# Performance work log

Hardware: AMD Instinct MI355X
Metric: run time of the kernel (lower is better)

The kernel has to match this reference:

```python
import jax, jax.numpy as jnp
import numpy as np

N = 100000
E = 1600000
NODE_DIM = 64
H = 128
NUM_LAYERS = 3
NUM_CLASSES = 6
NUM_GRAPHS = 512
LN_EPS = 1e-5


def setup_inputs() -> dict:
    key = jax.random.key(0)
    ks = jax.random.split(key, 16)
    s = 0.05
    x = jax.random.normal(ks[0], (N, NODE_DIM), jnp.float32)
    edge_index = jax.random.randint(ks[1], (2, E), 0, N, dtype=jnp.int64)
    batch = jnp.sort(jax.random.randint(ks[2], (N,), 0, NUM_GRAPHS, dtype=jnp.int64))
    return {
        "x": x,
        "edge_index": edge_index,
        "batch": batch,
        "proj_w": jax.random.normal(ks[3], (NODE_DIM, H), jnp.float32) * s,
        "proj_b": jnp.zeros((H,), jnp.float32),
        "lin_l_w": jax.random.normal(ks[4], (NUM_LAYERS, H, H), jnp.float32) * s,
        "lin_l_b": jnp.zeros((NUM_LAYERS, H), jnp.float32),
        "lin_r_w": jax.random.normal(ks[5], (NUM_LAYERS, H, H), jnp.float32) * s,
        "ln_g": jnp.ones((NUM_LAYERS, H), jnp.float32),
        "ln_b": jnp.zeros((NUM_LAYERS, H), jnp.float32),
        "gate_w1": jax.random.normal(ks[6], (H, H // 2), jnp.float32) * s,
        "gate_b1": jnp.zeros((H // 2,), jnp.float32),
        "gate_w2": jax.random.normal(ks[7], (H // 2, 1), jnp.float32) * s,
        "gate_b2": jnp.zeros((1,), jnp.float32),
        "cls_w1": jax.random.normal(ks[8], (H, H // 2), jnp.float32) * s,
        "cls_b1": jnp.zeros((H // 2,), jnp.float32),
        "cls_w2": jax.random.normal(ks[9], (H // 2, NUM_CLASSES), jnp.float32) * s,
        "cls_b2": jnp.zeros((NUM_CLASSES,), jnp.float32),
    }


def _layer_norm(x, g, b):
    mu = jnp.mean(x, axis=-1, keepdims=True)
    var = jnp.mean(jnp.square(x - mu), axis=-1, keepdims=True)
    return (x - mu) * jax.lax.rsqrt(var + LN_EPS) * g + b


def _sage_mean_aggr(x, src, dst):
    # mean of source node features grouped by destination node
    summed = jax.ops.segment_sum(x[src], dst, num_segments=N)  # [N,H]
    deg = jax.ops.segment_sum(jnp.ones((E,), x.dtype), dst, num_segments=N)
    return summed / jnp.maximum(deg, 1.0)[:, None]


def reference(x, edge_index, batch, proj_w, proj_b, lin_l_w, lin_l_b, lin_r_w,
              ln_g, ln_b, gate_w1, gate_b1, gate_w2, gate_b2,
              cls_w1, cls_b1, cls_w2, cls_b2):
    src, dst = edge_index[0], edge_index[1]
    h = jax.nn.relu(x @ proj_w + proj_b)  # [N,H]
    for l in range(NUM_LAYERS):
        r = h
        aggr = _sage_mean_aggr(h, src, dst)
        # PyG SAGEConv: lin_l(aggregated) + lin_r(self), bias only in lin_l
        h = aggr @ lin_l_w[l] + lin_l_b[l] + h @ lin_r_w[l]
        h = _layer_norm(h, ln_g[l], ln_b[l])
        h = jax.nn.elu(h)
        h = h + r  # dropout is identity in eval mode
    # GlobalAttention pooling: segment softmax over nodes per graph
    gate = (jax.nn.relu(h @ gate_w1 + gate_b1) @ gate_w2 + gate_b2)[:, 0]  # [N]
    gmax = jax.ops.segment_max(gate, batch, num_segments=NUM_GRAPHS)
    eg = jnp.exp(gate - gmax[batch])
    denom = jax.ops.segment_sum(eg, batch, num_segments=NUM_GRAPHS)
    alpha = eg / denom[batch]  # [N]
    pooled = jax.ops.segment_sum(h * alpha[:, None], batch, num_segments=NUM_GRAPHS)  # [G,H]
    out = jax.nn.relu(pooled @ cls_w1 + cls_b1) @ cls_w2 + cls_b2  # [G,C]
    return out
```

## Files before the change

### kernel.cpp

```cpp
#include <hip/hip_runtime.h>
#include <hip/hip_fp16.h>
#include <math.h>

#define N_NODES   100000
#define N_EDGES   1600000
#define NDIM      64
#define H         128
#define NUM_LAYERS 3
#define NUM_CLASSES 6
#define NUM_GRAPHS 512
#define LN_EPS    1e-5f
#define NBKT      391
#define SCAP      5376
#define BPAD      136

typedef _Float16 f16x8 __attribute__((ext_vector_type(8)));
typedef float    f32x4 __attribute__((ext_vector_type(4)));

__device__ __forceinline__ int idx_at(const int* raw, int is64, int i) {
    return is64 ? raw[2 * (long long)i] : raw[i];
}
__device__ __forceinline__ int lower_bound(const int* a, int n, int v) {
    int lo = 0, hi = n;
    while (lo < hi) { int m = (lo + hi) >> 1; if (a[m] < v) lo = m + 1; else hi = m; }
    return lo;
}

__device__ __forceinline__ f32x4 gload16(const __half* __restrict__ base, int voff) {
    f32x4 r;
    asm volatile("global_load_dwordx4 %0, %1, %2"
                 : "=v"(r) : "v"(voff), "s"(base));
    return r;
}

__global__ void k_detect(const int* eraw, const int* braw, int* flags,
                         int* bcnt, float* gate_z) {
    int i = blockIdx.x * blockDim.x + threadIdx.x;
    if (i < 512) bcnt[i] = 0;
    if (i < 64) gate_z[i] = 0.f;
    if (i == 0) {
        int e64 = 1;
        for (int k = 1; k < 128; k += 2) if (eraw[k] != 0) { e64 = 0; break; }
        flags[0] = e64;
        flags[1] = (braw[N_NODES - 1] == 0) ? 1 : 0;
    }
}

__global__ __launch_bounds__(256) void k_bhist(const int* eraw, const int* braw,
                                               const int* flags, int* bcnt, int* batch32) {
    __shared__ int c[512];
    int tid = threadIdx.x;
    for (int i = tid; i < 512; i += 256) c[i] = 0;
    __syncthreads();
    int f = flags[0];
    int gi = blockIdx.x * 256 + tid;
    if (gi < N_NODES) batch32[gi] = idx_at(braw, flags[1], gi);
    int stride = gridDim.x * 256;
    for (int e = blockIdx.x * 256 + tid; e < N_EDGES; e += stride) {
        int d = idx_at(eraw, f, N_EDGES + e);
        atomicAdd(&c[d >> 8], 1);
    }
    __syncthreads();
    for (int i = tid; i < 512; i += 256) if (c[i]) atomicAdd(&bcnt[i], c[i]);
}

__global__ void k_bscan(const int* bcnt, int* boff, int* bcursor) {
    __shared__ int sh[512];
    int tid = threadIdx.x;
    int v = bcnt[tid];
    sh[tid] = v;
    __syncthreads();
    for (int off = 1; off < 512; off <<= 1) {
        int u = (tid >= off) ? sh[tid - off] : 0;
        __syncthreads();
        sh[tid] += u;
        __syncthreads();
    }
    int excl = sh[tid] - v;
    boff[tid] = excl;
    bcursor[tid] = excl;
    if (tid == 511) boff[512] = sh[511];
}

#define EPB 4096
__global__ __launch_bounds__(256) void k_bucket(const int* eraw, const int* flags,
                                                int* bcursor, unsigned int* br) {
    __shared__ int cnt[512];
    __shared__ int excl[512];
    __shared__ int resv[512];
    __shared__ int lcur[512];
    __shared__ int psum[256];
    __shared__ unsigned int srec[EPB];
    __shared__ unsigned short sbkt[EPB];
    int tid = threadIdx.x;
    int f = flags[0];
    int base = blockIdx.x * EPB;
    int se[16], de[16];
#pragma unroll
    for (int j = 0; j < 16; ++j) {
        int e = base + j * 256 + tid;
        if (e < N_EDGES) {
            se[j] = idx_at(eraw, f, e);
            de[j] = idx_at(eraw, f, N_EDGES + e);
        } else de[j] = -1;
    }
    for (int i = tid; i < 512; i += 256) cnt[i] = 0;
    __syncthreads();
#pragma unroll
    for (int j = 0; j < 16; ++j)
        if (de[j] >= 0) atomicAdd(&cnt[de[j] >> 8], 1);
    __syncthreads();
    int b0 = cnt[2 * tid], b1 = cnt[2 * tid + 1];
    psum[tid] = b0 + b1;
    __syncthreads();
    for (int off = 1; off < 256; off <<= 1) {
        int u = (tid >= off) ? psum[tid - off] : 0;
        __syncthreads();
        psum[tid] += u;
        __syncthreads();
    }
    int pex = psum[tid] - (b0 + b1);
    excl[2 * tid] = pex;
    excl[2 * tid + 1] = pex + b0;
    lcur[2 * tid] = pex;
    lcur[2 * tid + 1] = pex + b0;
    resv[2 * tid]     = b0 ? atomicAdd(&bcursor[2 * tid], b0) : 0;
    resv[2 * tid + 1] = b1 ? atomicAdd(&bcursor[2 * tid + 1], b1) : 0;
    __syncthreads();
#pragma unroll
    for (int j = 0; j < 16; ++j)
        if (de[j] >= 0) {
            int b = de[j] >> 8;
            int slot = atomicAdd(&lcur[b], 1);
            srec[slot] = ((unsigned int)(de[j] & 255) << 24) | (unsigned int)se[j];
            sbkt[slot] = (unsigned short)b;
        }
    __syncthreads();
    int vtot = psum[255];
    for (int s2 = tid; s2 < vtot; s2 += 256) {
        int b = sbkt[s2];
        br[resv[b] + (s2 - excl[b])] = srec[s2];
    }
}

__global__ __launch_bounds__(256) void k_csr_tail(const unsigned int* br, const int* boff,
                                                  int* rowptr, int* col) {
    __shared__ int d256[256];
    __shared__ int sc[256];
    __shared__ int cbuf[SCAP];
    int b = blockIdx.x;
    int tid = threadIdx.x;
    int lo = boff[b], hi = boff[b + 1];
    int wsize = hi - lo;
    d256[tid] = 0;
    __syncthreads();
    for (int i = lo + tid; i < hi; i += 256)
        atomicAdd(&d256[br[i] >> 24], 1);
    __syncthreads();
    int v = d256[tid];
    sc[tid] = v;
    __syncthreads();
    for (int off = 1; off < 256; off <<= 1) {
        int u = (tid >= off) ? sc[tid - off] : 0;
        __syncthreads();
        sc[tid] += u;
        __syncthreads();
    }
    int excl = sc[tid] - v;
    int node = (b << 8) + tid;
    if (node < N_NODES) rowptr[node] = lo + excl;
    if (b == NBKT - 1 && tid == 0) rowptr[N_NODES] = N_EDGES;
    __syncthreads();
    d256[tid] = excl;
    __syncthreads();
    if (wsize <= SCAP) {
        for (int i = lo + tid; i < hi; i += 256) {
            unsigned int r = br[i];
            int p = atomicAdd(&d256[r >> 24], 1);
            cbuf[p] = (int)(r & 0xFFFFFF);
        }
        __syncthreads();
        for (int j = tid; j < wsize; j += 256) col[lo + j] = cbuf[j] << 8;
    } else {
        for (int i = lo + tid; i < hi; i += 256) {
            unsigned int r = br[i];
            int p = atomicAdd(&d256[r >> 24], 1);
            col[lo + p] = (int)(r & 0xFFFFFF) << 8;
        }
    }
}

__global__ void k_prepw(const float* __restrict__ lin_l_w, const float* __restrict__ lin_r_w,
                        const float* __restrict__ gate_w1,
                        __half* __restrict__ W16t, __half* __restrict__ W16g) {
    int i = blockIdx.x * 256 + threadIdx.x;
    if (i < NUM_LAYERS * 128 * 256) {
        int l = i >> 15;
        int rem = i & 32767;
        int n = rem >> 8;
        int k = rem & 255;
        float v = (k < 128) ? lin_l_w[(size_t)l * 16384 + k * 128 + n]
                            : lin_r_w[(size_t)l * 16384 + (k - 128) * 128 + n];
        W16t[(size_t)l * 32768 + n * 256 + k] = __float2half(v);
    } else if (i < NUM_LAYERS * 128 * 256 + 64 * 128) {
        int idx = i - NUM_LAYERS * 128 * 256;
        int n = idx >> 7;
        int k = idx & 127;
        W16g[n * 128 + k] = __float2half(gate_w1[k * 64 + n]);
    }
}

__global__ __launch_bounds__(256) void k_gemm_proj(const float* __restrict__ A,
                                                   const float* __restrict__ W,
                                                   const float* __restrict__ bias,
                                                   __half* __restrict__ C16,
                                                   int nrows, int K) {
    __shared__ float As_t[32][68];
    __shared__ float Ws[32 * 128];
    int tid = threadIdx.x;
    int row0 = blockIdx.x * 64;
    int tr = tid >> 4;
    int tc = tid & 15;
    int c0 = tc * 8;
    float acc[4][8];
#pragma unroll
    for (int i = 0; i < 4; ++i)
#pragma unroll
        for (int j = 0; j < 8; ++j) acc[i][j] = 0.f;

    for (int kc = 0; kc < K; kc += 32) {
        __syncthreads();
#pragma unroll
        for (int it = 0; it < 2; ++it) {
            int idx = tid + it * 256;
            int r = idx >> 3, c4 = idx & 7;
            int gr = row0 + r;
            float4 v = make_float4(0.f, 0.f, 0.f, 0.f);
            if (gr < nrows) v = *(const float4*)(A + (size_t)gr * K + kc + c4 * 4);
            As_t[c4 * 4 + 0][r] = v.x;
            As_t[c4 * 4 + 1][r] = v.y;
            As_t[c4 * 4 + 2][r] = v.z;
            As_t[c4 * 4 + 3][r] = v.w;
        }
#pragma unroll
        for (int it = 0; it < 4; ++it) {
            int idx = tid + it * 256;
            int r = idx >> 5, c4 = idx & 31;
            *(float4*)(&Ws[r * 128 + c4 * 4]) = *(const float4*)(W + (size_t)(kc + r) * 128 + c4 * 4);
        }
        __syncthreads();
#pragma unroll
        for (int k = 0; k < 32; ++k) {
            float4 a4 = *(const float4*)(&As_t[k][tr * 4]);
            float a[4] = {a4.x, a4.y, a4.z, a4.w};
            float4 w0 = *(const float4*)(&Ws[k * 128 + c0]);
            float4 w1 = *(const float4*)(&Ws[k * 128 + c0 + 4]);
            float w[8] = {w0.x, w0.y, w0.z, w0.w, w1.x, w1.y, w1.z, w1.w};
#pragma unroll
            for (int i = 0; i < 4; ++i)
#pragma unroll
                for (int j = 0; j < 8; ++j) acc[i][j] += a[i] * w[j];
        }
    }
    float bv[8];
#pragma unroll
    for (int j = 0; j < 8; ++j) bv[j] = bias[c0 + j];
#pragma unroll
    for (int i = 0; i < 4; ++i) {
        int gr = row0 + tr * 4 + i;
        if (gr < nrows) {
            float o[8];
#pragma unroll
            for (int j = 0; j < 8; ++j) o[j] = fmaxf(acc[i][j] + bv[j], 0.f);
            __half2 p[4];
#pragma unroll
            for (int j = 0; j < 8; j += 2) p[j / 2] = __floats2half2_rn(o[j], o[j + 1]);
            *(float4*)(C16 + (size_t)gr * 128 + c0) = *(float4*)p;
        }
    }
}

__global__ __launch_bounds__(256) void k_layer_mfma(const __half* __restrict__ t16,
                                                    __half* __restrict__ h16,
                                                    const __half* __restrict__ W16t,
                                                    const float* __restrict__ bl,
                                                    const float* __restrict__ g,
                                                    const float* __restrict__ bb) {
    __shared__ __half Bs[128 * BPAD];
    int tid = threadIdx.x;
    int wave = tid >> 6, lane = tid & 63;
    int s = lane & 15, quad = lane >> 4;
    int row0 = blockIdx.x * 64;
    int wrow0 = row0 + wave * 16;
    int arow = wrow0 + s;
    if (arow >= N_NODES) arow = N_NODES - 1;

    f32x4 acc[8];
#pragma unroll
    for (int c = 0; c < 8; ++c) acc[c] = (f32x4){0.f, 0.f, 0.f, 0.f};

#pragma unroll
    for (int ph = 0; ph < 2; ++ph) {
        __syncthreads();
#pragma unroll
        for (int it = 0; it < 8; ++it) {
            int idx = tid + it * 256;
            int n = idx >> 4, ch = idx & 15;
            *(float4*)(&Bs[n * BPAD + ch * 8]) =
                *(const float4*)(W16t + (size_t)n * 256 + ph * 128 + ch * 8);
        }
        __syncthreads();
        const __half* aptr = (ph ? h16 : t16) + (size_t)arow * H;
#pragma unroll
        for (int kk = 0; kk < 128; kk += 32) {
            f16x8 afrag = *(const f16x8*)(aptr + kk + quad * 8);
#pragma unroll
            for (int c = 0; c < 8; ++c) {
                f16x8 bfrag = *(const f16x8*)(&Bs[(c * 16 + s) * BPAD + kk + quad * 8]);
                acc[c] = __builtin_amdgcn_mfma_f32_16x16x32_f16(afrag, bfrag, acc[c], 0, 0, 0);
            }
        }
    }

    float y[8][4];
    float sm[4] = {0.f, 0.f, 0.f, 0.f}, sq[4] = {0.f, 0.f, 0.f, 0.f};
#pragma unroll
    for (int c = 0; c < 8; ++c) {
        float bv = bl[c * 16 + s];
#pragma unroll
        for (int i = 0; i < 4; ++i) {
            float v = acc[c][i] + bv;
            y[c][i] = v;
            sm[i] += v;
            sq[i] += v * v;
        }
    }
#pragma unroll
    for (int off = 1; off < 16; off <<= 1) {
#pragma unroll
        for (int i = 0; i < 4; ++i) {
            sm[i] += __shfl_xor(sm[i], off);
            sq[i] += __shfl_xor(sq[i], off);
        }
    }
    float mean[4], rstd[4];
#pragma unroll
    for (int i = 0; i < 4; ++i) {
        mean[i] = sm[i] * (1.0f / H);
        float var = sq[i] * (1.0f / H) - mean[i] * mean[i];
        rstd[i] = rsqrtf(var + LN_EPS);
    }
    float gv[8], bbv[8];
#pragma unroll
    for (int c = 0; c < 8; ++c) { gv[c] = g[c * 16 + s]; bbv[c] = bb[c * 16 + s]; }

    __syncthreads();
#pragma unroll
    for (int i = 0; i < 4; ++i) {
        int lr = wave * 16 + quad * 4 + i;
#pragma unroll
        for (int c = 0; c < 8; ++c) {
            float yv = (y[c][i] - mean[i]) * rstd[i] * gv[c] + bbv[c];
            yv = yv > 0.f ? yv : expf(yv) - 1.f;
            Bs[lr * BPAD + c * 16 + s] = __float2half(yv);
        }
    }
    __syncthreads();
#pragma unroll
    for (int it = 0; it < 4; ++it) {
        int idx = tid + it * 256;
        int r = idx >> 4, ch = idx & 15;
        int grow = row0 + r;
        if (grow < N_NODES) {
            float4 sv = *(float4*)(&Bs[r * BPAD + ch * 8]);
            float4 hv = *(const float4*)(h16 + (size_t)grow * H + ch * 8);
            __half2* pa = (__half2*)&sv;
            const __half2* pb = (const __half2*)&hv;
#pragma unroll
            for (int j = 0; j < 4; ++j) {
                float2 fa = __half22float2(pa[j]);
                float2 fb = __half22float2(pb[j]);
                pa[j] = __floats2half2_rn(fa.x + fb.x, fa.y + fb.y);
            }
            *(float4*)(h16 + (size_t)grow * H + ch * 8) = sv;
        }
    }
}

__global__ __launch_bounds__(256) void k_layer_gate(const __half* __restrict__ t16,
                                                    __half* __restrict__ h16,
                                                    const __half* __restrict__ W16t,
                                                    const float* __restrict__ bl,
                                                    const float* __restrict__ g,
                                                    const float* __restrict__ bb,
                                                    const __half* __restrict__ W16g,
                                                    const float* __restrict__ gb1,
                                                    const float* __restrict__ gw2,
                                                    const float* __restrict__ gb2,
                                                    float* __restrict__ gateout) {
    __shared__ __half Bs[128 * BPAD];
    int tid = threadIdx.x;
    int wave = tid >> 6, lane = tid & 63;
    int s = lane & 15, quad = lane >> 4;
    int row0 = blockIdx.x * 64;
    int wrow0 = row0 + wave * 16;
    int arow = wrow0 + s;
    if (arow >= N_NODES) arow = N_NODES - 1;

    f32x4 acc[8];
#pragma unroll
    for (int c = 0; c < 8; ++c) acc[c] = (f32x4){0.f, 0.f, 0.f, 0.f};

#pragma unroll
    for (int ph = 0; ph < 2; ++ph) {
        __syncthreads();
#pragma unroll
        for (int it = 0; it < 8; ++it) {
            int idx = tid + it * 256;
            int n = idx >> 4, ch = idx & 15;
            *(float4*)(&Bs[n * BPAD + ch * 8]) =
                *(const float4*)(W16t + (size_t)n * 256 + ph * 128 + ch * 8);
        }
        __syncthreads();
        const __half* aptr = (ph ? h16 : t16) + (size_t)arow * H;
#pragma unroll
        for (int kk = 0; kk < 128; kk += 32) {
            f16x8 afrag = *(const f16x8*)(aptr + kk + quad * 8);
#pragma unroll
            for (int c = 0; c < 8; ++c) {
                f16x8 bfrag = *(const f16x8*)(&Bs[(c * 16 + s) * BPAD + kk + quad * 8]);
                acc[c] = __builtin_amdgcn_mfma_f32_16x16x32_f16(afrag, bfrag, acc[c], 0, 0, 0);
            }
        }
    }

    float y[8][4];
    float sm[4] = {0.f, 0.f, 0.f, 0.f}, sq[4] = {0.f, 0.f, 0.f, 0.f};
#pragma unroll
    for (int c = 0; c < 8; ++c) {
        float bv = bl[c * 16 + s];
#pragma unroll
        for (int i = 0; i < 4; ++i) {
            float v = acc[c][i] + bv;
            y[c][i] = v;
            sm[i] += v;
            sq[i] += v * v;
        }
    }
#pragma unroll
    for (int off = 1; off < 16; off <<= 1) {
#pragma unroll
        for (int i = 0; i < 4; ++i) {
            sm[i] += __shfl_xor(sm[i], off);
            sq[i] += __shfl_xor(sq[i], off);
        }
    }
    float mean[4], rstd[4];
#pragma unroll
    for (int i = 0; i < 4; ++i) {
        mean[i] = sm[i] * (1.0f / H);
        float var = sq[i] * (1.0f / H) - mean[i] * mean[i];
        rstd[i] = rsqrtf(var + LN_EPS);
    }
    float gv[8], bbv[8];
#pragma unroll
    for (int c = 0; c < 8; ++c) { gv[c] = g[c * 16 + s]; bbv[c] = bb[c * 16 + s]; }

    __syncthreads();
#pragma unroll
    for (int i = 0; i < 4; ++i) {
        int lr = wave * 16 + quad * 4 + i;
#pragma unroll
        for (int c = 0; c < 8; ++c) {
            float yv = (y[c][i] - mean[i]) * rstd[i] * gv[c] + bbv[c];
            yv = yv > 0.f ? yv : expf(yv) - 1.f;
            Bs[lr * BPAD + c * 16 + s] = __float2half(yv);
        }
    }
    __syncthreads();
#pragma unroll
    for (int it = 0; it < 4; ++it) {
        int idx = tid + it * 256;
        int r = idx >> 4, ch = idx & 15;
        int grow = row0 + r;
        if (grow < N_NODES) {
            float4 sv = *(float4*)(&Bs[r * BPAD + ch * 8]);
            float4 hv = *(const float4*)(h16 + (size_t)grow * H + ch * 8);
            __half2* pa = (__half2*)&sv;
            const __half2* pb = (const __half2*)&hv;
#pragma unroll
            for (int j = 0; j < 4; ++j) {
                float2 fa = __half22float2(pa[j]);
                float2 fb = __half22float2(pb[j]);
                pa[j] = __floats2half2_rn(fa.x + fb.x, fa.y + fb.y);
            }
            *(float4*)(h16 + (size_t)grow * H + ch * 8) = sv;
        }
    }

    __syncthreads();
#pragma unroll
    for (int it = 0; it < 4; ++it) {
        int idx = tid + it * 256;
        int n = idx >> 4, ch = idx & 15;
        *(float4*)(&Bs[n * BPAD + ch * 8]) = *(const float4*)(W16g + (size_t)n * 128 + ch * 8);
    }
    __syncthreads();
    f32x4 gacc[4];
#pragma unroll
    for (int c = 0; c < 4; ++c) gacc[c] = (f32x4){0.f, 0.f, 0.f, 0.f};
    const __half* gaptr = h16 + (size_t)arow * H;
#pragma unroll
    for (int kc = 0; kc < 128; kc += 32) {
        f16x8 afrag = *(const f16x8*)(gaptr + kc + quad * 8);
#pragma unroll
        for (int c = 0; c < 4; ++c) {
            f16x8 bfrag = *(const f16x8*)(&Bs[(c * 16 + s) * BPAD + kc + quad * 8]);
            gacc[c] = __builtin_amdgcn_mfma_f32_16x16x32_f16(afrag, bfrag, gacc[c], 0, 0, 0);
        }
    }
    float part[4] = {0.f, 0.f, 0.f, 0.f};
#pragma unroll
    for (int c = 0; c < 4; ++c) {
        float bv = gb1[c * 16 + s];
        float wv = gw2[c * 16 + s];
#pragma unroll
        for (int i = 0; i < 4; ++i)
            part[i] += fmaxf(gacc[c][i] + bv, 0.f) * wv;
    }
#pragma unroll
    for (int off = 1; off < 16; off <<= 1) {
#pragma unroll
        for (int i = 0; i < 4; ++i) part[i] += __shfl_xor(part[i], off);
    }
    if (s == 0) {
        float b2v = gb2[0];
#pragma unroll
        for (int i = 0; i < 4; ++i) {
            int r = wrow0 + quad * 4 + i;
            if (r < N_NODES) gateout[r] = part[i] + b2v;
        }
    }
}

__global__ __launch_bounds__(256) void k_aggr(const __half* __restrict__ h16,
                                              const int* __restrict__ rowptr,
                                              const int* __restrict__ col,
                                              __half* __restrict__ t16,
                                              int zoff) {
    int lane = threadIdx.x & 63;
    int node = blockIdx.x * 4 + (threadIdx.x >> 6);
    if (node >= N_NODES) return;
    int s = lane & 15;
    int g = lane >> 4;
    int soff = s * 16;
    int e0 = rowptr[node];
    int deg = rowptr[node + 1] - e0;

    if (deg == 0) {
        if (g == 0) {
            float4 zz = make_float4(0.f, 0.f, 0.f, 0.f);
            *(float4*)(t16 + (size_t)node * H + s * 8) = zz;
        }
        return;
    }

    __half2 z = __floats2half2_rn(0.f, 0.f);
    __half2 ac[4][4];
#pragma unroll
    for (int a = 0; a < 4; ++a)
#pragma unroll
        for (int k = 0; k < 4; ++k) ac[a][k] = z;

    {
        int cb[8];
#pragma unroll
        for (int j = 0; j < 8; ++j) {
            int ei = g + 4 * j;
            cb[j] = col[e0 + (ei < deg ? ei : 0)];
        }
#pragma unroll
        for (int j = 0; j < 8; ++j) {
            int ei = g + 4 * j;
            cb[j] = ((ei < deg) ? cb[j] : zoff) + soff;
        }
        __builtin_amdgcn_sched_barrier(0);
        f32x4 rv[8];
#pragma unroll
        for (int j = 0; j < 8; ++j) rv[j] = gload16(h16, cb[j]);
        asm volatile("s_waitcnt vmcnt(0)" ::: "memory");
        __builtin_amdgcn_sched_barrier(0);
#pragma unroll
        for (int j = 0; j < 8; ++j) {
            const __half2* hv = (const __half2*)&rv[j];
            int a = j & 3;
            ac[a][0] = __hadd2(ac[a][0], hv[0]);
            ac[a][1] = __hadd2(ac[a][1], hv[1]);
            ac[a][2] = __hadd2(ac[a][2], hv[2]);
            ac[a][3] = __hadd2(ac[a][3], hv[3]);
        }
    }

    if (deg > 32) {
        for (int base = 32; base < deg; base += 32) {
            int cb[8];
#pragma unroll
            for (int j = 0; j < 8; ++j) {
                int ei = base + g + 4 * j;
                cb[j] = col[e0 + (ei < deg ? ei : base)];
            }
#pragma unroll
            for (int j = 0; j < 8; ++j) {
                int ei = base + g + 4 * j;
                cb[j] = ((ei < deg) ? cb[j] : zoff) + soff;
            }
            __builtin_amdgcn_sched_barrier(0);
            f32x4 rv[8];
#pragma unroll
            for (int j = 0; j < 8; ++j) rv[j] = gload16(h16, cb[j]);
            asm volatile("s_waitcnt vmcnt(0)" ::: "memory");
            __builtin_amdgcn_sched_barrier(0);
#pragma unroll
            for (int j = 0; j < 8; ++j) {
                const __half2* hv = (const __half2*)&rv[j];
                int a = j & 3;
                ac[a][0] = __hadd2(ac[a][0], hv[0]);
                ac[a][1] = __hadd2(ac[a][1], hv[1]);
                ac[a][2] = __hadd2(ac[a][2], hv[2]);
                ac[a][3] = __hadd2(ac[a][3], hv[3]);
            }
        }
    }

    float f[8];
#pragma unroll
    for (int k = 0; k < 4; ++k) {
        float2 s0 = __half22float2(ac[0][k]);
        float2 s1 = __half22float2(ac[1][k]);
        float2 s2 = __half22float2(ac[2][k]);
        float2 s3 = __half22float2(ac[3][k]);
        f[2 * k]     = (s0.x + s1.x) + (s2.x + s3.x);
        f[2 * k + 1] = (s0.y + s1.y) + (s2.y + s3.y);
    }
#pragma unroll
    for (int off = 16; off <= 32; off <<= 1) {
#pragma unroll
        for (int k = 0; k < 8; ++k) f[k] += __shfl_xor(f[k], off);
    }
    if (g == 0) {
        float inv = 1.0f / (float)(deg > 1 ? deg : 1);
        __half2 o[4];
#pragma unroll
        for (int k = 0; k < 4; ++k)
            o[k] = __floats2half2_rn(f[2 * k] * inv, f[2 * k + 1] * inv);
        *(float4*)(t16 + (size_t)node * H + s * 8) = *(float4*)o;
    }
}

__global__ __launch_bounds__(256) void k_smx_pool_cls(const __half* __restrict__ h16,
                                                      const float* __restrict__ gatein,
                                                      const int* __restrict__ batch32,
                                                      const float* __restrict__ w1,
                                                      const float* __restrict__ b1,
                                                      const float* __restrict__ w2,
                                                      const float* __restrict__ b2,
                                                      float* __restrict__ out) {
    __shared__ float seg[512];
    __shared__ float red[256];
    __shared__ float smem[256 * 8];
    __shared__ float sp[64];
    int g = blockIdx.x;
    int tid = threadIdx.x;
    int n0 = lower_bound(batch32, N_NODES, g);
    int n1 = lower_bound(batch32, N_NODES, g + 1);
    int cnt = n1 - n0;
    int cc = cnt < 512 ? cnt : 512;

    float g0 = (tid < cc) ? gatein[n0 + tid] : -INFINITY;
    float g1 = (256 + tid < cc) ? gatein[n0 + 256 + tid] : -INFINITY;
    red[tid] = fmaxf(g0, g1);
    __syncthreads();
    for (int st = 128; st >= 1; st >>= 1) {
        if (tid < st) red[tid] = fmaxf(red[tid], red[tid + st]);
        __syncthreads();
    }
    float m = red[0];
    __syncthreads();
    float e0 = (tid < cc) ? expf(g0 - m) : 0.f;
    float e1 = (256 + tid < cc) ? expf(g1 - m) : 0.f;
    if (tid < cc) seg[tid] = e0;
    if (256 + tid < cc) seg[256 + tid] = e1;
    red[tid] = e0 + e1;
    __syncthreads();
    for (int st = 128; st >= 1; st >>= 1) {
        if (tid < st) red[tid] += red[tid + st];
        __syncthreads();
    }
    float gs = red[0];
    __syncthreads();

    int c8 = tid & 15, p = tid >> 4;
    float f[8];
#pragma unroll
    for (int j = 0; j < 8; ++j) f[j] = 0.f;
    for (int ln = p; ln < cc; ln += 16) {
        float4 v = *(const float4*)(h16 + (size_t)(n0 + ln) * H + c8 * 8);
        const __half2* hv = (const __half2*)&v;
        float w = seg[ln];
#pragma unroll
        for (int j = 0; j < 4; ++j) {
            float2 fv = __half22float2(hv[j]);
            f[2 * j]     += w * fv.x;
            f[2 * j + 1] += w * fv.y;
        }
    }
#pragma unroll
    for (int j = 0; j < 8; ++j) smem[tid * 8 + j] = f[j];
    __syncthreads();
    for (int st = 8; st >= 1; st >>= 1) {
        if (p < st) {
#pragma unroll
            for (int j = 0; j < 8; ++j)
                smem[tid * 8 + j] += smem[(tid + st * 16) * 8 + j];
        }
        __syncthreads();
    }
    if (p == 0) {
#pragma unroll
        for (int j = 0; j < 8; ++j)
            red[c8 * 8 + j] = (cnt > 0) ? smem[c8 * 8 + j] / gs : 0.f;
    }
    __syncthreads();

    if (tid < 64) {
        float r0 = red[tid];
        float r1 = red[64 + tid];
        float acc = b1[tid];
#pragma unroll 16
        for (int k = 0; k < 64; ++k) acc += __shfl(r0, k) * w1[k * 64 + tid];
#pragma unroll 16
        for (int k = 0; k < 64; ++k) acc += __shfl(r1, k) * w1[(64 + k) * 64 + tid];
        sp[tid] = fmaxf(acc, 0.f);
    }
    __syncthreads();
    if (tid < NUM_CLASSES) {
        float o = b2[tid];
        for (int c = 0; c < 64; ++c) o += sp[c] * w2[c * NUM_CLASSES + tid];
        out[g * NUM_CLASSES + tid] = o;
    }
}

extern "C" void kernel_launch(void* const* d_in, const int* in_sizes, int n_in,
                              void* d_out, int out_size, void* d_ws, size_t ws_size,
                              hipStream_t stream) {
    const float* x       = (const float*)d_in[0];
    const int*   eraw    = (const int*)d_in[1];
    const int*   braw    = (const int*)d_in[2];
    const float* proj_w  = (const float*)d_in[3];
    const float* proj_b  = (const float*)d_in[4];
    const float* lin_l_w = (const float*)d_in[5];
    const float* lin_l_b = (const float*)d_in[6];
    const float* lin_r_w = (const float*)d_in[7];
    const float* ln_g    = (const float*)d_in[8];
    const float* ln_b    = (const float*)d_in[9];
    const float* gate_w1 = (const float*)d_in[10];
    const float* gate_b1 = (const float*)d_in[11];
    const float* gate_w2 = (const float*)d_in[12];
    const float* gate_b2 = (const float*)d_in[13];
    const float* cls_w1  = (const float*)d_in[14];
    const float* cls_b1  = (const float*)d_in[15];
    const float* cls_w2  = (const float*)d_in[16];
    const float* cls_b2  = (const float*)d_in[17];
    float* out = (float*)d_out;

    __half* h16    = (__half*)d_ws;
    __half* t16    = h16 + (size_t)N_NODES * H;
    float*  gate   = (float*)(t16 + (size_t)N_NODES * H);
    float*  gsum   = gate + N_NODES;
    float*  pooled = gsum + NUM_GRAPHS;
    __half* W16t   = (__half*)(pooled + NUM_GRAPHS * H);
    __half* W16g   = W16t + (size_t)NUM_LAYERS * 32768;
    int* flags     = (int*)(W16g + 64 * 128);
    int* col       = flags + 4;
    int* batch32   = col + N_EDGES;
    int* rowptr    = batch32 + N_NODES;
    int* bcnt      = rowptr + N_NODES + 1;
    int* boff      = bcnt + 512;
    int* bcursor   = boff + 513;
    unsigned int* br = (unsigned int*)(bcursor + 512);

    const int zoff = (int)((const char*)gate - (const char*)h16);

    const int nbE4 = (N_EDGES + EPB - 1) / EPB;
    const int nbW = (N_NODES + 3) / 4;
    const int nbG = (N_NODES + 63) / 64;
    const int nbP = (NUM_LAYERS * 128 * 256 + 64 * 128 + 255) / 256;

    k_detect<<<2, 256, 0, stream>>>(eraw, braw, flags, bcnt, gate);
    k_bhist<<<512, 256, 0, stream>>>(eraw, braw, flags, bcnt, batch32);
    k_bscan<<<1, 512, 0, stream>>>(bcnt, boff, bcursor);
    k_bucket<<<nbE4, 256, 0, stream>>>(eraw, flags, bcursor, br);
    k_csr_tail<<<NBKT, 256, 0, stream>>>(br, boff, rowptr, col);
    k_prepw<<<nbP, 256, 0, stream>>>(lin_l_w, lin_r_w, gate_w1, W16t, W16g);

    k_gemm_proj<<<nbG, 256, 0, stream>>>(x, proj_w, proj_b, h16, N_NODES, NDIM);

    for (int l = 0; l < NUM_LAYERS; ++l) {
        const float* bl  = lin_l_b + (size_t)l * H;
        const float* gl  = ln_g + (size_t)l * H;
        const float* blb = ln_b + (size_t)l * H;
        k_aggr<<<nbW, 256, 0, stream>>>(h16, rowptr, col, t16, zoff);
        if (l < NUM_LAYERS - 1) {
            k_layer_mfma<<<nbG, 256, 0, stream>>>(t16, h16, W16t + (size_t)l * 32768, bl, gl, blb);
        } else {
            k_layer_gate<<<nbG, 256, 0, stream>>>(t16, h16, W16t + (size_t)l * 32768, bl, gl, blb,
                                                  W16g, gate_b1, gate_w2, gate_b2, gate);
        }
    }

    k_smx_pool_cls<<<NUM_GRAPHS, 256, 0, stream>>>(h16, gate, batch32,
                                                   cls_w1, cls_b1, cls_w2, cls_b2, out);
}
```

Before: 457.7 us.

## Store node features in column-sliced planar layout and slice aggregation by feature chunk

New measurement: 608.6 us. 1.33x slower.

```diff
diff --git a/kernel.cpp b/kernel.cpp
--- a/kernel.cpp
+++ b/kernel.cpp
@@ -13,6 +13,7 @@
 #define NBKT      391
 #define SCAP      5376
 #define BPAD      136
+#define PLH32     (N_NODES * 16)
 
 typedef _Float16 f16x8 __attribute__((ext_vector_type(8)));
 typedef float    f32x4 __attribute__((ext_vector_type(4)));
@@ -25,10 +26,13 @@
     while (lo < hi) { int m = (lo + hi) >> 1; if (a[m] < v) lo = m + 1; else hi = m; }
     return lo;
 }
-
-__device__ __forceinline__ f32x4 gload16(const __half* __restrict__ base, int voff) {
-    f32x4 r;
-    asm volatile("global_load_dwordx4 %0, %1, %2"
+__device__ __forceinline__ size_t pmoff(int c, int n) {
+    return (size_t)(c >> 1) * PLH32 + (size_t)n * 16 + (size_t)((c & 1) * 8);
+}
+
+__device__ __forceinline__ float2 gload8(const __half* __restrict__ base, int voff) {
+    float2 r;
+    asm volatile("global_load_dwordx2 %0, %1, %2"
                  : "=v"(r) : "v"(voff), "s"(base));
     return r;
 }
@@ -180,12 +184,12 @@
             cbuf[p] = (int)(r & 0xFFFFFF);
         }
         __syncthreads();
-        for (int j = tid; j < wsize; j += 256) col[lo + j] = cbuf[j] << 8;
+        for (int j = tid; j < wsize; j += 256) col[lo + j] = cbuf[j] << 5;
     } else {
         for (int i = lo + tid; i < hi; i += 256) {
             unsigned int r = br[i];
             int p = atomicAdd(&d256[r >> 24], 1);
-            col[lo + p] = (int)(r & 0xFFFFFF) << 8;
+            col[lo + p] = (int)(r & 0xFFFFFF) << 5;
         }
     }
 }
@@ -275,7 +279,7 @@
             __half2 p[4];
 #pragma unroll
             for (int j = 0; j < 8; j += 2) p[j / 2] = __floats2half2_rn(o[j], o[j + 1]);
-            *(float4*)(C16 + (size_t)gr * 128 + c0) = *(float4*)p;
+            *(float4*)(C16 + pmoff(tc, gr)) = *(float4*)p;
         }
     }
 }
@@ -310,10 +314,10 @@
                 *(const float4*)(W16t + (size_t)n * 256 + ph * 128 + ch * 8);
         }
         __syncthreads();
-        const __half* aptr = (ph ? h16 : t16) + (size_t)arow * H;
+        const __half* aptr = ph ? h16 : t16;
 #pragma unroll
         for (int kk = 0; kk < 128; kk += 32) {
-            f16x8 afrag = *(const f16x8*)(aptr + kk + quad * 8);
+            f16x8 afrag = *(const f16x8*)(aptr + pmoff(kk / 8 + quad, arow));
 #pragma unroll
             for (int c = 0; c < 8; ++c) {
                 f16x8 bfrag = *(const f16x8*)(&Bs[(c * 16 + s) * BPAD + kk + quad * 8]);
@@ -369,11 +373,11 @@
 #pragma unroll
     for (int it = 0; it < 4; ++it) {
         int idx = tid + it * 256;
-        int r = idx >> 4, ch = idx & 15;
+        int r = idx & 63, ch = idx >> 6;
         int grow = row0 + r;
         if (grow < N_NODES) {
             float4 sv = *(float4*)(&Bs[r * BPAD + ch * 8]);
-            float4 hv = *(const float4*)(h16 + (size_t)grow * H + ch * 8);
+            float4 hv = *(const float4*)(h16 + pmoff(ch, grow));
             __half2* pa = (__half2*)&sv;
             const __half2* pb = (const __half2*)&hv;
 #pragma unroll
@@ -382,7 +386,7 @@
                 float2 fb = __half22float2(pb[j]);
                 pa[j] = __floats2half2_rn(fa.x + fb.x, fa.y + fb.y);
             }
-            *(float4*)(h16 + (size_t)grow * H + ch * 8) = sv;
+            *(float4*)(h16 + pmoff(ch, grow)) = sv;
         }
     }
 }
@@ -422,10 +426,10 @@
                 *(const float4*)(W16t + (size_t)n * 256 + ph * 128 + ch * 8);
         }
         __syncthreads();
-        const __half* aptr = (ph ? h16 : t16) + (size_t)arow * H;
+        const __half* aptr = ph ? h16 : t16;
 #pragma unroll
         for (int kk = 0; kk < 128; kk += 32) {
-            f16x8 afrag = *(const f16x8*)(aptr + kk + quad * 8);
+            f16x8 afrag = *(const f16x8*)(aptr + pmoff(kk / 8 + quad, arow));
 #pragma unroll
             for (int c = 0; c < 8; ++c) {
                 f16x8 bfrag = *(const f16x8*)(&Bs[(c * 16 + s) * BPAD + kk + quad * 8]);
@@ -481,11 +485,11 @@
 #pragma unroll
     for (int it = 0; it < 4; ++it) {
         int idx = tid + it * 256;
-        int r = idx >> 4, ch = idx & 15;
+        int r = idx & 63, ch = idx >> 6;
         int grow = row0 + r;
         if (grow < N_NODES) {
             float4 sv = *(float4*)(&Bs[r * BPAD + ch * 8]);
-            float4 hv = *(const float4*)(h16 + (size_t)grow * H + ch * 8);
+            float4 hv = *(const float4*)(h16 + pmoff(ch, grow));
             __half2* pa = (__half2*)&sv;
             const __half2* pb = (const __half2*)&hv;
 #pragma unroll
@@ -494,7 +498,7 @@
                 float2 fb = __half22float2(pb[j]);
                 pa[j] = __floats2half2_rn(fa.x + fb.x, fa.y + fb.y);
             }
-            *(float4*)(h16 + (size_t)grow * H + ch * 8) = sv;
+            *(float4*)(h16 + pmoff(ch, grow)) = sv;
         }
     }
 
@@ -509,10 +513,9 @@
     f32x4 gacc[4];
 #pragma unroll
     for (int c = 0; c < 4; ++c) gacc[c] = (f32x4){0.f, 0.f, 0.f, 0.f};
-    const __half* gaptr = h16 + (size_t)arow * H;
 #pragma unroll
     for (int kc = 0; kc < 128; kc += 32) {
-        f16x8 afrag = *(const f16x8*)(gaptr + kc + quad * 8);
+        f16x8 afrag = *(const f16x8*)(h16 + pmoff(kc / 8 + quad, arow));
 #pragma unroll
         for (int c = 0; c < 4; ++c) {
             f16x8 bfrag = *(const f16x8*)(&Bs[(c * 16 + s) * BPAD + kc + quad * 8]);
@@ -548,112 +551,104 @@
                                               const int* __restrict__ col,
                                               __half* __restrict__ t16,
                                               int zoff) {
-    int lane = threadIdx.x & 63;
-    int node = blockIdx.x * 4 + (threadIdx.x >> 6);
-    if (node >= N_NODES) return;
-    int s = lane & 15;
-    int g = lane >> 4;
-    int soff = s * 16;
-    int e0 = rowptr[node];
-    int deg = rowptr[node + 1] - e0;
-
-    if (deg == 0) {
-        if (g == 0) {
-            float4 zz = make_float4(0.f, 0.f, 0.f, 0.f);
-            *(float4*)(t16 + (size_t)node * H + s * 8) = zz;
-        }
-        return;
-    }
-
-    __half2 z = __floats2half2_rn(0.f, 0.f);
-    __half2 ac[4][4];
-#pragma unroll
-    for (int a = 0; a < 4; ++a)
-#pragma unroll
-        for (int k = 0; k < 4; ++k) ac[a][k] = z;
-
-    {
-        int cb[8];
-#pragma unroll
-        for (int j = 0; j < 8; ++j) {
-            int ei = g + 4 * j;
-            cb[j] = col[e0 + (ei < deg ? ei : 0)];
-        }
-#pragma unroll
-        for (int j = 0; j < 8; ++j) {
-            int ei = g + 4 * j;
-            cb[j] = ((ei < deg) ? cb[j] : zoff) + soff;
-        }
+    int tid = threadIdx.x;
+    int slice = blockIdx.x & 7;
+    int nb = blockIdx.x >> 3;
+    int lane = tid & 63;
+    int e = lane >> 2, q = lane & 3;
+    int pq = slice * (N_NODES * 32) + q * 8;
+    char* tb = (char*)t16 + slice * (N_NODES * 32) + q * 8;
+    int nbase = nb * 256 + (tid >> 6) * 64;
+
+    for (int itn = 0; itn < 16; ++itn) {
+        int n0 = nbase + itn * 4;
+        if (n0 >= N_NODES) return;
+        int4 rp = *(const int4*)(rowptr + n0);
+        int rp4 = rowptr[n0 + 4];
+        int d0 = rp.y - rp.x, d1 = rp.z - rp.y, d2 = rp.w - rp.z, d3 = rp4 - rp.w;
+        int i0 = e, i1 = 16 + e;
+        int c0 = col[rp.x + (i0 < d0 ? i0 : 0)];
+        int c1 = col[rp.x + (i1 < d0 ? i1 : 0)];
+        int c2 = col[rp.y + (i0 < d1 ? i0 : 0)];
+        int c3 = col[rp.y + (i1 < d1 ? i1 : 0)];
+        int c4 = col[rp.z + (i0 < d2 ? i0 : 0)];
+        int c5 = col[rp.z + (i1 < d2 ? i1 : 0)];
+        int c6 = col[rp.w + (i0 < d3 ? i0 : 0)];
+        int c7 = col[rp.w + (i1 < d3 ? i1 : 0)];
+        int v0 = (i0 < d0) ? c0 + pq : zoff;
+        int v1 = (i1 < d0) ? c1 + pq : zoff;
+        int v2 = (i0 < d1) ? c2 + pq : zoff;
+        int v3 = (i1 < d1) ? c3 + pq : zoff;
+        int v4 = (i0 < d2) ? c4 + pq : zoff;
+        int v5 = (i1 < d2) ? c5 + pq : zoff;
+        int v6 = (i0 < d3) ? c6 + pq : zoff;
+        int v7 = (i1 < d3) ? c7 + pq : zoff;
         __builtin_amdgcn_sched_barrier(0);
-        f32x4 rv[8];
-#pragma unroll
-        for (int j = 0; j < 8; ++j) rv[j] = gload16(h16, cb[j]);
+        float2 g0 = gload8(h16, v0);
+        float2 g1 = gload8(h16, v1);
+        float2 g2 = gload8(h16, v2);
+        float2 g3 = gload8(h16, v3);
+        float2 g4 = gload8(h16, v4);
+        float2 g5 = gload8(h16, v5);
+        float2 g6 = gload8(h16, v6);
+        float2 g7 = gload8(h16, v7);
         asm volatile("s_waitcnt vmcnt(0)" ::: "memory");
         __builtin_amdgcn_sched_barrier(0);
-#pragma unroll
-        for (int j = 0; j < 8; ++j) {
-            const __half2* hv = (const __half2*)&rv[j];
-            int a = j & 3;
-            ac[a][0] = __hadd2(ac[a][0], hv[0]);
-            ac[a][1] = __hadd2(ac[a][1], hv[1]);
-            ac[a][2] = __hadd2(ac[a][2], hv[2]);
-            ac[a][3] = __hadd2(ac[a][3], hv[3]);
-        }
-    }
-
-    if (deg > 32) {
-        for (int base = 32; base < deg; base += 32) {
-            int cb[8];
-#pragma unroll
-            for (int j = 0; j < 8; ++j) {
-                int ei = base + g + 4 * j;
-                cb[j] = col[e0 + (ei < deg ? ei : base)];
+
+        __half2 al[4], ah[4];
+        {
+            const __half2* p0 = (const __half2*)&g0;
+            const __half2* p1 = (const __half2*)&g1;
+            al[0] = __hadd2(p0[0], p1[0]); ah[0] = __hadd2(p0[1], p1[1]);
+            const __half2* p2 = (const __half2*)&g2;
+            const __half2* p3 = (const __half2*)&g3;
+            al[1] = __hadd2(p2[0], p3[0]); ah[1] = __hadd2(p2[1], p3[1]);
+            const __half2* p4 = (const __half2*)&g4;
+            const __half2* p5 = (const __half2*)&g5;
+            al[2] = __hadd2(p4[0], p5[0]); ah[2] = __hadd2(p4[1], p5[1]);
+            const __half2* p6 = (const __half2*)&g6;
+            const __half2* p7 = (const __half2*)&g7;
+            al[3] = __hadd2(p6[0], p7[0]); ah[3] = __hadd2(p6[1], p7[1]);
+        }
+
+        if ((d0 > 32) | (d1 > 32) | (d2 > 32) | (d3 > 32)) {
+            int dd0[4] = {d0, d1, d2, d3};
+            int ee0[4] = {rp.x, rp.y, rp.z, rp.w};
+#pragma unroll
+            for (int j = 0; j < 4; ++j) {
+                for (int base = 32; base < dd0[j]; base += 16) {
+                    int ii = base + e;
+                    int cc = col[ee0[j] + (ii < dd0[j] ? ii : 0)];
+                    int vv = (ii < dd0[j]) ? cc + pq : zoff;
+                    float2 gg = gload8(h16, vv);
+                    asm volatile("s_waitcnt vmcnt(0)" ::: "memory");
+                    const __half2* pg = (const __half2*)&gg;
+                    al[j] = __hadd2(al[j], pg[0]);
+                    ah[j] = __hadd2(ah[j], pg[1]);
+                }
             }
-#pragma unroll
-            for (int j = 0; j < 8; ++j) {
-                int ei = base + g + 4 * j;
-                cb[j] = ((ei < deg) ? cb[j] : zoff) + soff;
+        }
+
+        int dd[4] = {d0, d1, d2, d3};
+#pragma unroll
+        for (int j = 0; j < 4; ++j) {
+#pragma unroll
+            for (int off = 4; off <= 32; off <<= 1) {
+                int tl = __shfl_xor(*(int*)&al[j], off);
+                int th = __shfl_xor(*(int*)&ah[j], off);
+                al[j] = __hadd2(al[j], *(__half2*)&tl);
+                ah[j] = __hadd2(ah[j], *(__half2*)&th);
             }
-            __builtin_amdgcn_sched_barrier(0);
-            f32x4 rv[8];
-#pragma unroll
-            for (int j = 0; j < 8; ++j) rv[j] = gload16(h16, cb[j]);
-            asm volatile("s_waitcnt vmcnt(0)" ::: "memory");
-            __builtin_amdgcn_sched_barrier(0);
-#pragma unroll
-            for (int j = 0; j < 8; ++j) {
-                const __half2* hv = (const __half2*)&rv[j];
-                int a = j & 3;
-                ac[a][0] = __hadd2(ac[a][0], hv[0]);
-                ac[a][1] = __hadd2(ac[a][1], hv[1]);
-                ac[a][2] = __hadd2(ac[a][2], hv[2]);
-                ac[a][3] = __hadd2(ac[a][3], hv[3]);
+            if (e == 0) {
+                float2 fl = __half22float2(al[j]);
+                float2 fh = __half22float2(ah[j]);
+                float inv = 1.0f / (float)(dd[j] > 1 ? dd[j] : 1);
+                float2 ov;
+                ((__half2*)&ov)[0] = __floats2half2_rn(fl.x * inv, fl.y * inv);
+                ((__half2*)&ov)[1] = __floats2half2_rn(fh.x * inv, fh.y * inv);
+                *(float2*)(tb + (size_t)(n0 + j) * 32) = ov;
             }
         }
-    }
-
-    float f[8];
-#pragma unroll
-    for (int k = 0; k < 4; ++k) {
-        float2 s0 = __half22float2(ac[0][k]);
-        float2 s1 = __half22float2(ac[1][k]);
-        float2 s2 = __half22float2(ac[2][k]);
-        float2 s3 = __half22float2(ac[3][k]);
-        f[2 * k]     = (s0.x + s1.x) + (s2.x + s3.x);
-        f[2 * k + 1] = (s0.y + s1.y) + (s2.y + s3.y);
-    }
-#pragma unroll
-    for (int off = 16; off <= 32; off <<= 1) {
-#pragma unroll
-        for (int k = 0; k < 8; ++k) f[k] += __shfl_xor(f[k], off);
-    }
-    if (g == 0) {
-        float inv = 1.0f / (float)(deg > 1 ? deg : 1);
-        __half2 o[4];
-#pragma unroll
-        for (int k = 0; k < 4; ++k)
-            o[k] = __floats2half2_rn(f[2 * k] * inv, f[2 * k + 1] * inv);
-        *(float4*)(t16 + (size_t)node * H + s * 8) = *(float4*)o;
     }
 }
 
@@ -704,7 +699,7 @@
 #pragma unroll
     for (int j = 0; j < 8; ++j) f[j] = 0.f;
     for (int ln = p; ln < cc; ln += 16) {
-        float4 v = *(const float4*)(h16 + (size_t)(n0 + ln) * H + c8 * 8);
+        float4 v = *(const float4*)(h16 + pmoff(c8, n0 + ln));
         const __half2* hv = (const __half2*)&v;
         float w = seg[ln];
 #pragma unroll
@@ -792,7 +787,7 @@
     const int zoff = (int)((const char*)gate - (const char*)h16);
 
     const int nbE4 = (N_EDGES + EPB - 1) / EPB;
-    const int nbW = (N_NODES + 3) / 4;
+    const int nbA = 8 * NBKT;
     const int nbG = (N_NODES + 63) / 64;
     const int nbP = (NUM_LAYERS * 128 * 256 + 64 * 128 + 255) / 256;
 
@@ -809,7 +804,7 @@
         const float* bl  = lin_l_b + (size_t)l * H;
         const float* gl  = ln_g + (size_t)l * H;
         const float* blb = ln_b + (size_t)l * H;
-        k_aggr<<<nbW, 256, 0, stream>>>(h16, rowptr, col, t16, zoff);
+        k_aggr<<<nbA, 256, 0, stream>>>(h16, rowptr, col, t16, zoff);
         if (l < NUM_LAYERS - 1) {
             k_layer_mfma<<<nbG, 256, 0, stream>>>(t16, h16, W16t + (size_t)l * 32768, bl, gl, blb);
         } else {
```

## Replace edge histogram and scan with fixed-capacity destination buckets

Applied to the files above, without the earlier changes.

Result: faster. 435.6 us, median of 2 (-4.8%).

```diff
diff --git a/kernel.cpp b/kernel.cpp
--- a/kernel.cpp
+++ b/kernel.cpp
@@ -11,6 +11,7 @@
 #define NUM_GRAPHS 512
 #define LN_EPS    1e-5f
 #define NBKT      391
+#define BCAP      4608
 #define SCAP      5376
 #define BPAD      136
 
@@ -34,9 +35,9 @@
 }
 
 __global__ void k_detect(const int* eraw, const int* braw, int* flags,
-                         int* bcnt, float* gate_z) {
+                         int* bcursor, float* gate_z) {
     int i = blockIdx.x * blockDim.x + threadIdx.x;
-    if (i < 512) bcnt[i] = 0;
+    if (i < 512) bcursor[i] = i * BCAP;
     if (i < 64) gate_z[i] = 0.f;
     if (i == 0) {
         int e64 = 1;
@@ -46,45 +47,11 @@
     }
 }
 
-__global__ __launch_bounds__(256) void k_bhist(const int* eraw, const int* braw,
-                                               const int* flags, int* bcnt, int* batch32) {
-    __shared__ int c[512];
-    int tid = threadIdx.x;
-    for (int i = tid; i < 512; i += 256) c[i] = 0;
-    __syncthreads();
-    int f = flags[0];
-    int gi = blockIdx.x * 256 + tid;
-    if (gi < N_NODES) batch32[gi] = idx_at(braw, flags[1], gi);
-    int stride = gridDim.x * 256;
-    for (int e = blockIdx.x * 256 + tid; e < N_EDGES; e += stride) {
-        int d = idx_at(eraw, f, N_EDGES + e);
-        atomicAdd(&c[d >> 8], 1);
-    }
-    __syncthreads();
-    for (int i = tid; i < 512; i += 256) if (c[i]) atomicAdd(&bcnt[i], c[i]);
-}
-
-__global__ void k_bscan(const int* bcnt, int* boff, int* bcursor) {
-    __shared__ int sh[512];
-    int tid = threadIdx.x;
-    int v = bcnt[tid];
-    sh[tid] = v;
-    __syncthreads();
-    for (int off = 1; off < 512; off <<= 1) {
-        int u = (tid >= off) ? sh[tid - off] : 0;
-        __syncthreads();
-        sh[tid] += u;
-        __syncthreads();
-    }
-    int excl = sh[tid] - v;
-    boff[tid] = excl;
-    bcursor[tid] = excl;
-    if (tid == 511) boff[512] = sh[511];
-}
-
 #define EPB 4096
-__global__ __launch_bounds__(256) void k_bucket(const int* eraw, const int* flags,
-                                                int* bcursor, unsigned int* br) {
+__global__ __launch_bounds__(256) void k_bucket(const int* eraw, const int* braw,
+                                                const int* flags,
+                                                int* bcursor, unsigned int* br,
+                                                int* batch32) {
     __shared__ int cnt[512];
     __shared__ int excl[512];
     __shared__ int resv[512];
@@ -95,6 +62,8 @@
     int tid = threadIdx.x;
     int f = flags[0];
     int base = blockIdx.x * EPB;
+    int gi = blockIdx.x * 256 + tid;
+    if (gi < N_NODES) batch32[gi] = idx_at(braw, flags[1], gi);
     int se[16], de[16];
 #pragma unroll
     for (int j = 0; j < 16; ++j) {
@@ -143,14 +112,14 @@
     }
 }
 
-__global__ __launch_bounds__(256) void k_csr_tail(const unsigned int* br, const int* boff,
-                                                  int* rowptr, int* col) {
+__global__ __launch_bounds__(256) void k_csr_tail(const unsigned int* br, const int* bcursor,
+                                                  int* rowptr, int* degarr, int* col) {
     __shared__ int d256[256];
     __shared__ int sc[256];
     __shared__ int cbuf[SCAP];
     int b = blockIdx.x;
     int tid = threadIdx.x;
-    int lo = boff[b], hi = boff[b + 1];
+    int lo = b * BCAP, hi = bcursor[b];
     int wsize = hi - lo;
     d256[tid] = 0;
     __syncthreads();
@@ -168,8 +137,10 @@
     }
     int excl = sc[tid] - v;
     int node = (b << 8) + tid;
-    if (node < N_NODES) rowptr[node] = lo + excl;
-    if (b == NBKT - 1 && tid == 0) rowptr[N_NODES] = N_EDGES;
+    if (node < N_NODES) {
+        rowptr[node] = lo + excl;
+        degarr[node] = v;
+    }
     __syncthreads();
     d256[tid] = excl;
     __syncthreads();
@@ -545,6 +516,7 @@
 
 __global__ __launch_bounds__(256) void k_aggr(const __half* __restrict__ h16,
                                               const int* __restrict__ rowptr,
+                                              const int* __restrict__ degarr,
                                               const int* __restrict__ col,
                                               __half* __restrict__ t16,
                                               int zoff) {
@@ -555,7 +527,7 @@
     int g = lane >> 4;
     int soff = s * 16;
     int e0 = rowptr[node];
-    int deg = rowptr[node + 1] - e0;
+    int deg = degarr[node];
 
     if (deg == 0) {
         if (g == 0) {
@@ -776,17 +748,14 @@
     __half* h16    = (__half*)d_ws;
     __half* t16    = h16 + (size_t)N_NODES * H;
     float*  gate   = (float*)(t16 + (size_t)N_NODES * H);
-    float*  gsum   = gate + N_NODES;
-    float*  pooled = gsum + NUM_GRAPHS;
-    __half* W16t   = (__half*)(pooled + NUM_GRAPHS * H);
+    __half* W16t   = (__half*)(gate + N_NODES);
     __half* W16g   = W16t + (size_t)NUM_LAYERS * 32768;
     int* flags     = (int*)(W16g + 64 * 128);
     int* col       = flags + 4;
-    int* batch32   = col + N_EDGES;
+    int* batch32   = col + 512 * BCAP;
     int* rowptr    = batch32 + N_NODES;
-    int* bcnt      = rowptr + N_NODES + 1;
-    int* boff      = bcnt + 512;
-    int* bcursor   = boff + 513;
+    int* degarr    = rowptr + N_NODES;
+    int* bcursor   = degarr + N_NODES;
     unsigned int* br = (unsigned int*)(bcursor + 512);
 
     const int zoff = (int)((const char*)gate - (const char*)h16);
@@ -796,11 +765,9 @@
     const int nbG = (N_NODES + 63) / 64;
     const int nbP = (NUM_LAYERS * 128 * 256 + 64 * 128 + 255) / 256;
 
-    k_detect<<<2, 256, 0, stream>>>(eraw, braw, flags, bcnt, gate);
-    k_bhist<<<512, 256, 0, stream>>>(eraw, braw, flags, bcnt, batch32);
-    k_bscan<<<1, 512, 0, stream>>>(bcnt, boff, bcursor);
-    k_bucket<<<nbE4, 256, 0, stream>>>(eraw, flags, bcursor, br);
-    k_csr_tail<<<NBKT, 256, 0, stream>>>(br, boff, rowptr, col);
+    k_detect<<<2, 256, 0, stream>>>(eraw, braw, flags, bcursor, gate);
+    k_bucket<<<nbE4, 256, 0, stream>>>(eraw, braw, flags, bcursor, br, batch32);
+    k_csr_tail<<<NBKT, 256, 0, stream>>>(br, bcursor, rowptr, degarr, col);
     k_prepw<<<nbP, 256, 0, stream>>>(lin_l_w, lin_r_w, gate_w1, W16t, W16g);
 
     k_gemm_proj<<<nbG, 256, 0, stream>>>(x, proj_w, proj_b, h16, N_NODES, NDIM);
@@ -809,7 +776,7 @@
         const float* bl  = lin_l_b + (size_t)l * H;
         const float* gl  = ln_g + (size_t)l * H;
         const float* blb = ln_b + (size_t)l * H;
-        k_aggr<<<nbW, 256, 0, stream>>>(h16, rowptr, col, t16, zoff);
+        k_aggr<<<nbW, 256, 0, stream>>>(h16, rowptr, degarr, col, t16, zoff);
         if (l < NUM_LAYERS - 1) {
             k_layer_mfma<<<nbG, 256, 0, stream>>>(t16, h16, W16t + (size_t)l * 32768, bl, gl, blb);
         } else {
```
